# Kernel optimization log

Hardware: AMD Instinct MI355X
Metric: run time of the kernel (lower is better)

## Reference

```python
import jax, jax.numpy as jnp
import numpy as np

N, E = 50000, 800000
F_NODE, F_EDGE, H, LAT, MAXN = 128, 16, 128, 64, 200


def setup_inputs() -> dict:
    key = jax.random.key(0)
    ks = jax.random.split(key, 40)
    s = 0.05
    p = {
        'x': jax.random.normal(ks[0], (N, F_NODE), jnp.float32),
        'edge_index': jax.random.randint(ks[1], (2, E), 0, N, jnp.int64),
        'edge_attr': jax.random.normal(ks[2], (E, F_EDGE), jnp.float32),
        'eps': jax.random.normal(ks[3], (1, LAT), jnp.float32),
        'num_nodes': N,
        # GATConv layer 1 (heads=1)
        'W1': jax.random.normal(ks[4], (F_NODE, H), jnp.float32) * s,
        'att_src1': jax.random.normal(ks[5], (H,), jnp.float32) * s,
        'att_dst1': jax.random.normal(ks[6], (H,), jnp.float32) * s,
        'We1': jax.random.normal(ks[7], (F_EDGE, H), jnp.float32) * s,
        'att_e1': jax.random.normal(ks[8], (H,), jnp.float32) * s,
        'b1': jnp.zeros((H,), jnp.float32),
        # GATConv layer 2
        'W2': jax.random.normal(ks[9], (H, H), jnp.float32) * s,
        'att_src2': jax.random.normal(ks[10], (H,), jnp.float32) * s,
        'att_dst2': jax.random.normal(ks[11], (H,), jnp.float32) * s,
        'We2': jax.random.normal(ks[12], (F_EDGE, H), jnp.float32) * s,
        'att_e2': jax.random.normal(ks[13], (H,), jnp.float32) * s,
        'b2': jnp.zeros((H,), jnp.float32),
        # heads
        'mu_W': jax.random.normal(ks[14], (H, LAT), jnp.float32) * s,
        'mu_b': jnp.zeros((LAT,), jnp.float32),
        'lv_W': jax.random.normal(ks[15], (H, LAT), jnp.float32) * s,
        'lv_b': jnp.zeros((LAT,), jnp.float32),
        'dec_W': jax.random.normal(ks[16], (LAT, H), jnp.float32) * s,
        'dec_b': jnp.zeros((H,), jnp.float32),
        'adj_W1': jax.random.normal(ks[17], (H, H), jnp.float32) * s,
        'adj_b1': jnp.zeros((H,), jnp.float32),
        'adj_W2': jax.random.normal(ks[18], (H, MAXN), jnp.float32) * s,
        'adj_b2': jnp.zeros((MAXN,), jnp.float32),
        'nd_W1': jax.random.normal(ks[19], (H, H), jnp.float32) * s,
        'nd_b1': jnp.zeros((H,), jnp.float32),
        'nd_W2': jax.random.normal(ks[20], (H, F_NODE), jnp.float32) * s,
        'nd_b2': jnp.zeros((F_NODE,), jnp.float32),
    }
    return p


def _gat(h, src, dst, ea, W, a_s, a_d, We, a_e, b, n):
    # PyG GATConv, heads=1: linear transform, per-edge attention, segment softmax over dst
    g = h @ W                                     # [n, H]
    alpha = jax.nn.leaky_relu((g @ a_s)[src] + (g @ a_d)[dst] + (ea @ We) @ a_e,
                              negative_slope=0.2)  # [E']
    m = jax.ops.segment_max(alpha, dst, num_segments=n)
    ex = jnp.exp(alpha - m[dst])
    den = jax.ops.segment_sum(ex, dst, num_segments=n)
    w = ex / den[dst]
    return jax.ops.segment_sum(w[:, None] * g[src], dst, num_segments=n) + b


def _forward(x, edge_index, edge_attr, eps, num_nodes,
             W1, att_src1, att_dst1, We1, att_e1, b1,
             W2, att_src2, att_dst2, We2, att_e2, b2,
             mu_W, mu_b, lv_W, lv_b, dec_W, dec_b,
             adj_W1, adj_b1, adj_W2, adj_b2, nd_W1, nd_b1, nd_W2, nd_b2):
    n = x.shape[0]
    src, dst = edge_index[0], edge_index[1]
    # add self loops; self-loop edge_attr = per-node mean of incoming edge_attr (PyG fill_value='mean')
    deg = jax.ops.segment_sum(jnp.ones((src.shape[0],), x.dtype), dst, num_segments=n)
    mean_ea = jax.ops.segment_sum(edge_attr, dst, num_segments=n) / jnp.maximum(deg, 1.0)[:, None]
    loop = jnp.arange(n)
    src_f = jnp.concatenate([src, loop])
    dst_f = jnp.concatenate([dst, loop])
    ea_f = jnp.concatenate([edge_attr, mean_ea])
    h = jax.nn.relu(_gat(x, src_f, dst_f, ea_f, W1, att_src1, att_dst1, We1, att_e1, b1, n))
    h = jax.nn.relu(_gat(h, src_f, dst_f, ea_f, W2, att_src2, att_dst2, We2, att_e2, b2, n))
    hg = h.mean(axis=0, keepdims=True)            # global_mean_pool, single graph -> [1, H]
    mu = hg @ mu_W + mu_b
    logvar = hg @ lv_W + lv_b
    z = mu + eps * jnp.exp(0.5 * logvar)
    hd = jax.nn.relu(z @ dec_W + dec_b)           # [1, H]
    hn = jnp.broadcast_to(hd[:, None, :], (1, num_nodes, hd.shape[-1]))
    adj = jax.nn.relu(hn @ adj_W1 + adj_b1) @ adj_W2 + adj_b2   # [1, n, MAXN]
    adj = adj[:, :, :num_nodes]
    nodes = jax.nn.relu(hn @ nd_W1 + nd_b1) @ nd_W2 + nd_b2     # [1, n, F_NODE]
    return adj, nodes, mu, logvar


def reference(x, edge_index, edge_attr, eps, num_nodes,
              W1, att_src1, att_dst1, We1, att_e1, b1,
              W2, att_src2, att_dst2, We2, att_e2, b2,
              mu_W, mu_b, lv_W, lv_b, dec_W, dec_b,
              adj_W1, adj_b1, adj_W2, adj_b2, nd_W1, nd_b1, nd_W2, nd_b2):
    return _forward(x, edge_index, edge_attr, eps, num_nodes,
                    W1, att_src1, att_dst1, We1, att_e1, b1,
                    W2, att_src2, att_dst2, We2, att_e2, b2,
                    mu_W, mu_b, lv_W, lv_b, dec_W, dec_b,
                    adj_W1, adj_b1, adj_W2, adj_b2, nd_W1, nd_b1, nd_W2, nd_b2)
```

## Files before the change

kernel.cpp:

```cpp
#include <hip/hip_runtime.h>
#include <math.h>

#define NN   50000
#define EE   800000
#define EF   850000
#define HH   128
#define FE   16
#define LATD 64
#define MAXNN 200

#define ADJ_TOT   10000000
#define NODES_TOT 6400000
#define OUT_TOT   16400000
#define MU_OFF    16400000
#define LV_OFF    16400064

#define GEMMBLOCKS 782
#define DEGBLOCKS  782
#define NBSCAN     49

typedef __attribute__((ext_vector_type(8))) short bf16x8;
typedef __attribute__((ext_vector_type(4))) float f32x4;
typedef __attribute__((ext_vector_type(2))) float f32x2;

__device__ __forceinline__ unsigned short f2bf(float f){
  unsigned int u = __float_as_uint(f);
  unsigned int r = (u + 0x7FFFu + ((u>>16)&1u)) >> 16;
  return (unsigned short)r;
}
__device__ __forceinline__ float bf2f(unsigned short h){
  return __uint_as_float(((unsigned int)h)<<16);
}

__global__ __launch_bounds__(256) void kprep(int* ideg, float* hgsum,
                       const float* We1, const float* ae1, const float* We2, const float* ae2,
                       float* wa1, float* wa2,
                       const float* W1, const float* W2,
                       unsigned short* Wp1, unsigned short* Wp2){
  int i = blockIdx.x*256 + threadIdx.x;
  if(i < NN) ideg[i]=0;
  if(i < HH) hgsum[i]=0.f;
  if(i < FE){
    float s1=0.f, s2=0.f;
    for(int j=0;j<HH;j++){ s1 += We1[i*HH+j]*ae1[j]; s2 += We2[i*HH+j]*ae2[j]; }
    wa1[i]=s1; wa2[i]=s2;
  }
  if(i < HH*HH){
    int n = i >> 7, k = i & 127;
    Wp1[i] = f2bf(W1[k*HH + n]);
    Wp2[i] = f2bf(W2[k*HH + n]);
  }
}

__device__ __forceinline__ void gemm_body(int bid, int tid, const void* __restrict__ hin, int h_is_fp32,
    const unsigned short* __restrict__ Wp,
    const float* __restrict__ atts, const float* __restrict__ attd,
    unsigned char* __restrict__ A8, float* __restrict__ asrc, float* __restrict__ adst){
  int lane = tid & 63;
  int wid  = tid >> 6;
  int l = lane & 15, q = lane >> 4;
  int r0 = bid*64 + wid*16;
  if(r0 >= NN) return;
  const unsigned short* hb = (const unsigned short*)hin;
  const float*          hf = (const float*)hin;
  int row = r0 + l;

  bf16x8 afr[4];
  if(h_is_fp32){
    float4 u[8];
    #pragma unroll
    for(int kb=0;kb<4;kb++){
      const float* p = hf + (size_t)row*HH + kb*32 + q*8;
      u[kb*2]   = *(const float4*)(p);
      u[kb*2+1] = *(const float4*)(p+4);
    }
    #pragma unroll
    for(int kb=0;kb<4;kb++){
      afr[kb][0]=(short)f2bf(u[kb*2].x);   afr[kb][1]=(short)f2bf(u[kb*2].y);
      afr[kb][2]=(short)f2bf(u[kb*2].z);   afr[kb][3]=(short)f2bf(u[kb*2].w);
      afr[kb][4]=(short)f2bf(u[kb*2+1].x); afr[kb][5]=(short)f2bf(u[kb*2+1].y);
      afr[kb][6]=(short)f2bf(u[kb*2+1].z); afr[kb][7]=(short)f2bf(u[kb*2+1].w);
    }
  } else {
    #pragma unroll
    for(int kb=0;kb<4;kb++)
      afr[kb] = *(const bf16x8*)(hb + (size_t)row*HH + kb*32 + q*8);
  }

  f32x4 acc[8];
  #pragma unroll
  for(int t=0;t<8;t++) acc[t]=(f32x4){0.f,0.f,0.f,0.f};

  #pragma unroll
  for(int kb=0;kb<4;kb++){
    #pragma unroll
    for(int t=0;t<8;t++){
      bf16x8 b = *(const bf16x8*)(Wp + (size_t)(t*16+l)*HH + kb*32 + q*8);
      acc[t] = __builtin_amdgcn_mfma_f32_16x16x32_bf16(afr[kb], b, acc[t], 0,0,0);
    }
  }

  float av[8], dv[8];
  #pragma unroll
  for(int t=0;t<8;t++){ av[t]=atts[t*16+l]; dv[t]=attd[t*16+l]; }
  #pragma unroll
  for(int reg=0;reg<4;reg++){
    float ps=0.f, pd=0.f;
    #pragma unroll
    for(int t=0;t<8;t++){ ps+=acc[t][reg]*av[t]; pd+=acc[t][reg]*dv[t]; }
    #pragma unroll
    for(int m=8;m>=1;m>>=1){ ps+=__shfl_xor(ps,m,16); pd+=__shfl_xor(pd,m,16); }
    if(l==0){ int R=r0+q*4+reg; asrc[R]=ps; adst[R]=pd; }
  }
  #pragma unroll
  for(int t=0;t<8;t++)
    #pragma unroll
    for(int reg=0;reg<4;reg++){
      int pk = __builtin_amdgcn_cvt_pk_fp8_f32(acc[t][reg], 0.f, 0, false);
      A8[(size_t)(r0+q*4+reg)*HH + t*16 + l] = (unsigned char)(pk & 0xFF);
    }
}

__global__ __launch_bounds__(256) void kgemm3(const void* __restrict__ hin, int h_is_fp32,
    const unsigned short* __restrict__ Wp,
    const float* __restrict__ atts, const float* __restrict__ attd,
    unsigned char* __restrict__ A8, float* __restrict__ asrc, float* __restrict__ adst){
  gemm_body(blockIdx.x, threadIdx.x, hin, h_is_fp32, Wp, atts, attd, A8, asrc, adst);
}

__global__ __launch_bounds__(256) void kdeggemm(
    const int* __restrict__ ei, int* ideg, unsigned short* __restrict__ erank,
    const void* __restrict__ hin, int h_is_fp32,
    const unsigned short* __restrict__ Wp,
    const float* __restrict__ atts, const float* __restrict__ attd,
    unsigned char* __restrict__ A8, float* __restrict__ asrc, float* __restrict__ adst){
  if(blockIdx.x < GEMMBLOCKS){
    gemm_body(blockIdx.x, threadIdx.x, hin, h_is_fp32, Wp, atts, attd, A8, asrc, adst);
  } else {
    int e0 = ((blockIdx.x - GEMMBLOCKS)*256 + threadIdx.x)*4;
    if(e0 + 3 < EE){
      int4 d4 = *(const int4*)(ei + EE + e0);
      unsigned short r0 = (unsigned short)atomicAdd(&ideg[d4.x], 1);
      unsigned short r1 = (unsigned short)atomicAdd(&ideg[d4.y], 1);
      unsigned short r2 = (unsigned short)atomicAdd(&ideg[d4.z], 1);
      unsigned short r3 = (unsigned short)atomicAdd(&ideg[d4.w], 1);
      ushort4 rr; rr.x=r0; rr.y=r1; rr.z=r2; rr.w=r3;
      *(ushort4*)(erank + e0) = rr;
    } else {
      for(int j=0;j<4;j++)
        if(e0+j < EE) erank[e0+j] = (unsigned short)atomicAdd(&ideg[ei[EE+e0+j]], 1);
    }
  }
}

__global__ void kscan1(const int* __restrict__ ideg, int* rowstart, int* blocksum){
  __shared__ int sd[1024];
  int t=threadIdx.x; int i=blockIdx.x*1024+t;
  int v = (i<NN)? (ideg[i]+1) : 0;
  sd[t]=v; __syncthreads();
  for(int off=1; off<1024; off<<=1){
    int x = (t>=off)? sd[t-off] : 0;
    __syncthreads();
    sd[t] += x;
    __syncthreads();
  }
  if(i<NN) rowstart[i] = sd[t]-v;
  if(t==1023) blocksum[blockIdx.x]=sd[1023];
}
__global__ __launch_bounds__(256) void kscan3i(int* rowstart, const int* __restrict__ blocksum){
  __shared__ int bo[64];
  int t = threadIdx.x;
  if(t < 64){
    int v = (t < NBSCAN)? blocksum[t] : 0;
    int inc = v;
    #pragma unroll
    for(int off=1; off<64; off<<=1){
      int x = __shfl_up(inc, off);
      if(t>=off) inc += x;
    }
    bo[t] = inc - v;
  }
  __syncthreads();
  int i = blockIdx.x*256 + t;
  if(i<NN) rowstart[i] += bo[i>>10];
  if(i==0) rowstart[NN] = bo[NBSCAN];
}

__device__ __forceinline__ unsigned etpack(const float4* a4,
                         const float* __restrict__ wa1, const float* __restrict__ wa2){
  float4 v0=a4[0], v1=a4[1], v2=a4[2], v3=a4[3];
  float va[16]={v0.x,v0.y,v0.z,v0.w, v1.x,v1.y,v1.z,v1.w,
                v2.x,v2.y,v2.z,v2.w, v3.x,v3.y,v3.z,v3.w};
  float d1=0.f,d2=0.f;
  #pragma unroll
  for(int f=0;f<FE;f++){ d1+=va[f]*wa1[f]; d2+=va[f]*wa2[f]; }
  return (unsigned)f2bf(d1) | ((unsigned)f2bf(d2)<<16);
}
__global__ __launch_bounds__(256) void kscatter(const int* __restrict__ ei, const float* __restrict__ ea,
                         const float* __restrict__ wa1, const float* __restrict__ wa2,
                         const int* __restrict__ rowstart, const unsigned short* __restrict__ erank,
                         uint2* __restrict__ csr){
  int e0 = (blockIdx.x*256 + threadIdx.x)*2;
  if(e0>=EE) return;
  int sA=ei[e0],    sB=ei[e0+1];
  int dA=ei[EE+e0], dB=ei[EE+e0+1];
  int rA=(int)erank[e0], rB=(int)erank[e0+1];
  int pA=rowstart[dA]+rA, pB=rowstart[dB]+rB;
  const float4* a4 = (const float4*)(ea + (size_t)e0*FE);
  unsigned yA = etpack(a4,   wa1, wa2);
  unsigned yB = etpack(a4+4, wa1, wa2);
  uint2 enA; enA.x=(unsigned)sA; enA.y=yA;
  uint2 enB; enB.x=(unsigned)sB; enB.y=yB;
  csr[pA]=enA; csr[pB]=enB;
}

__global__ __launch_bounds__(256) void kgat(const unsigned char* __restrict__ A8,
    const float* __restrict__ asrc, const float* __restrict__ adst,
    const int* __restrict__ rowstart, uint2* __restrict__ csr,
    int mode, const float* __restrict__ bias,
    float* __restrict__ alphabuf, int* __restrict__ srcbuf,
    unsigned short* __restrict__ Bout){
  int lane = threadIdx.x & 63;
  int wid  = threadIdx.x >> 6;
  int half = lane >> 5;
  int hl   = lane & 31;
  int i = blockIdx.x*8 + wid*2 + half;
  if(i >= NN) return;
  int base = rowstart[i];
  int len  = rowstart[i+1]-base;
  float adi = adst[i];
  int lq = hl & 15;
  int qq = hl >> 4;
  float av[8];
  #pragma unroll
  for(int j=0;j<8;j++) av[j]=0.f;

  if(__builtin_expect(len <= 32, 1)){
    int P2 = (len+1)>>1;
    int nread = mode ? len : len-1;
    int s = i; float etlo = 0.f, ethi = 0.f;
    if(hl < nread){
      uint2 en = csr[base+hl];
      s = (int)en.x;
      etlo = bf2f((unsigned short)(en.y & 0xFFFFu));
      ethi = bf2f((unsigned short)(en.y >> 16));
    }
    float et = mode ? ethi : etlo;
    int skv0[6];
    #pragma unroll
    for(int j=0;j<6;j++) skv0[j] = (j<P2) ? __shfl(s, 2*j+qq, 32) : i;
    unsigned ux[6], uy[6];
    #pragma unroll
    for(int j=0;j<6;j++){
      uint2 u = *(const uint2*)(A8 + (size_t)skv0[j]*HH + lq*8);
      ux[j]=u.x; uy[j]=u.y;
    }
    if(!mode){
      float e1 = (hl < len-1) ? etlo : 0.f;
      float e2 = (hl < len-1) ? ethi : 0.f;
      #pragma unroll
      for(int mk=16;mk>=1;mk>>=1){ e1 += __shfl_xor(e1,mk); e2 += __shfl_xor(e2,mk); }
      float dg = fmaxf((float)(len-1), 1.f);
      float m1 = e1/dg, m2 = e2/dg;
      if(hl == len-1){
        et = m1;
        uint2 se; se.x=(unsigned)i;
        se.y=(unsigned)f2bf(m1) | ((unsigned)f2bf(m2)<<16);
        csr[base+len-1] = se;
      }
    }
    float a = -1e30f;
    if(hl < len){
      a = asrc[s] + adi + et;
      a = fmaxf(a, 0.2f*a);
    }
    float m = a;
    #pragma unroll
    for(int mk=16;mk>=1;mk>>=1) m = fmaxf(m, __shfl_xor(m,mk));
    float ex = (hl<len) ? __expf(a-m) : 0.f;
    float sm = ex;
    #pragma unroll
    for(int mk=16;mk>=1;mk>>=1) sm += __shfl_xor(sm,mk);
    ex *= __builtin_amdgcn_rcpf(sm);

    float w0[6];
    #pragma unroll
    for(int j=0;j<6;j++) w0[j] = (j<P2) ? __shfl(ex, 2*j+qq, 32) : 0.f;
    #pragma unroll
    for(int j=0;j<6;j++){
      f32x2 v;
      v=__builtin_amdgcn_cvt_pk_f32_fp8((int)ux[j],false); av[0]+=w0[j]*v[0]; av[1]+=w0[j]*v[1];
      v=__builtin_amdgcn_cvt_pk_f32_fp8((int)ux[j],true ); av[2]+=w0[j]*v[0]; av[3]+=w0[j]*v[1];
      v=__builtin_amdgcn_cvt_pk_f32_fp8((int)uy[j],false); av[4]+=w0[j]*v[0]; av[5]+=w0[j]*v[1];
      v=__builtin_amdgcn_cvt_pk_f32_fp8((int)uy[j],true ); av[6]+=w0[j]*v[0]; av[7]+=w0[j]*v[1];
    }
    for(int t0=6; t0<P2; t0+=6){
      int skv[6]; float w[6];
      #pragma unroll
      for(int j=0;j<6;j++){
        if(t0+j < P2){
          int idx = 2*(t0+j) + qq;
          skv[j] = __shfl(s, idx, 32);
          w[j]   = __shfl(ex, idx, 32);
        } else { skv[j] = i; w[j] = 0.f; }
      }
      unsigned vx[6], vy[6];
      #pragma unroll
      for(int j=0;j<6;j++){
        uint2 u = *(const uint2*)(A8 + (size_t)skv[j]*HH + lq*8);
        vx[j]=u.x; vy[j]=u.y;
      }
      #pragma unroll
      for(int j=0;j<6;j++){
        f32x2 v;
        v=__builtin_amdgcn_cvt_pk_f32_fp8((int)vx[j],false); av[0]+=w[j]*v[0]; av[1]+=w[j]*v[1];
        v=__builtin_amdgcn_cvt_pk_f32_fp8((int)vx[j],true ); av[2]+=w[j]*v[0]; av[3]+=w[j]*v[1];
        v=__builtin_amdgcn_cvt_pk_f32_fp8((int)vy[j],false); av[4]+=w[j]*v[0]; av[5]+=w[j]*v[1];
        v=__builtin_amdgcn_cvt_pk_f32_fp8((int)vy[j],true ); av[6]+=w[j]*v[0]; av[7]+=w[j]*v[1];
      }
    }
  } else {
    int deg = len-1;
    int lim = mode ? len : deg;
    float lm = -1e30f, e1 = 0.f, e2 = 0.f;
    for(int k=hl;k<lim;k+=32){
      uint2 en = csr[base+k];
      int sr = (int)en.x;
      float lo = bf2f((unsigned short)(en.y & 0xFFFFu));
      float hi = bf2f((unsigned short)(en.y >> 16));
      float etv = mode ? hi : lo;
      if(!mode){ e1 += lo; e2 += hi; }
      float a = asrc[sr] + adi + etv;
      a = fmaxf(a, 0.2f*a);
      alphabuf[base+k]=a; srcbuf[base+k]=sr;
      lm = fmaxf(lm,a);
    }
    #pragma unroll
    for(int mk=16;mk>=1;mk>>=1){
      e1 += __shfl_xor(e1,mk);
      e2 += __shfl_xor(e2,mk);
      lm  = fmaxf(lm, __shfl_xor(lm,mk));
    }
    float aself = 0.f;
    if(!mode){
      float m1 = e1/(float)deg, m2 = e2/(float)deg;
      aself = asrc[i] + adi + m1;
      aself = fmaxf(aself, 0.2f*aself);
      lm = fmaxf(lm, aself);
      if(hl==0){
        uint2 se; se.x=(unsigned)i;
        se.y=(unsigned)f2bf(m1) | ((unsigned)f2bf(m2)<<16);
        csr[base+deg] = se;
      }
    }
    float ls=0.f;
    for(int k=hl;k<len;k+=32){
      float a;
      if(mode) a = alphabuf[base+k];
      else     a = (k<deg)? alphabuf[base+k] : aself;
      float e_ = __expf(a-lm);
      alphabuf[base+k]=e_;
      ls += e_;
    }
    #pragma unroll
    for(int mk=16;mk>=1;mk>>=1) ls += __shfl_xor(ls,mk);
    float inv = 1.f/ls;
    int lim2 = mode ? len : deg;
    int P2 = (len+1)>>1;
    for(int t=0;t<P2;t++){
      int k = 2*t + qq;
      int sk = i; float wk = 0.f;
      if(k<len){
        sk = (k<lim2)? srcbuf[base+k] : i;
        wk = alphabuf[base+k]*inv;
      }
      uint2 u = *(const uint2*)(A8 + (size_t)sk*HH + lq*8);
      f32x2 v;
      v=__builtin_amdgcn_cvt_pk_f32_fp8((int)u.x,false); av[0]+=wk*v[0]; av[1]+=wk*v[1];
      v=__builtin_amdgcn_cvt_pk_f32_fp8((int)u.x,true ); av[2]+=wk*v[0]; av[3]+=wk*v[1];
      v=__builtin_amdgcn_cvt_pk_f32_fp8((int)u.y,false); av[4]+=wk*v[0]; av[5]+=wk*v[1];
      v=__builtin_amdgcn_cvt_pk_f32_fp8((int)u.y,true ); av[6]+=wk*v[0]; av[7]+=wk*v[1];
    }
  }

  #pragma unroll
  for(int j=0;j<8;j++) av[j] += __shfl_xor(av[j],16);
  if(qq==0){
    const float4* bp = (const float4*)(bias + lq*8);
    float4 b0=bp[0], b1=bp[1];
    float o0=fmaxf(av[0]+b0.x,0.f), o1=fmaxf(av[1]+b0.y,0.f);
    float o2=fmaxf(av[2]+b0.z,0.f), o3=fmaxf(av[3]+b0.w,0.f);
    float o4=fmaxf(av[4]+b1.x,0.f), o5=fmaxf(av[5]+b1.y,0.f);
    float o6=fmaxf(av[6]+b1.z,0.f), o7=fmaxf(av[7]+b1.w,0.f);
    uint4 ov;
    ov.x=(unsigned)f2bf(o0)|((unsigned)f2bf(o1)<<16);
    ov.y=(unsigned)f2bf(o2)|((unsigned)f2bf(o3)<<16);
    ov.z=(unsigned)f2bf(o4)|((unsigned)f2bf(o5)<<16);
    ov.w=(unsigned)f2bf(o6)|((unsigned)f2bf(o7)<<16);
    *(uint4*)(Bout + (size_t)i*HH + lq*8) = ov;
  }
}

__global__ __launch_bounds__(256) void khg(const unsigned short* __restrict__ B, float* hgsum){
  int f = threadIdx.x & 127;
  int half = threadIdx.x >> 7;
  float s=0.f;
  for(int i = blockIdx.x*2+half; i < NN; i += gridDim.x*2)
    s += bf2f(B[(size_t)i*HH + f]);
  __shared__ float sd[256];
  sd[threadIdx.x]=s; __syncthreads();
  if(half==0) atomicAdd(&hgsum[f], sd[threadIdx.x]+sd[threadIdx.x+128]);
}

__global__ __launch_bounds__(256) void kdec(const float* __restrict__ hgsum, const float* __restrict__ eps,
   const float* muW,const float* mub,const float* lvW,const float* lvb,
   const float* decW,const float* decb,
   const float* aW1,const float* ab1,const float* aW2,const float* ab2,
   const float* nW1,const float* nb1,const float* nW2,const float* nb2,
   float* out, float* rowadj, float* rownodes){
  __shared__ float hg[HH], z[LATD], hd[HH], t1[HH], t2[HH];
  int t=threadIdx.x;
  if(t<HH) hg[t]=hgsum[t]*(1.0f/NN);
  __syncthreads();
  if(t<LATD){
    float mu=mub[t], lv=lvb[t];
    #pragma unroll 8
    for(int k=0;k<HH;k++){ mu += hg[k]*muW[k*LATD+t]; lv += hg[k]*lvW[k*LATD+t]; }
    out[MU_OFF+t]=mu; out[LV_OFF+t]=lv;
    z[t]=mu + eps[t]*expf(0.5f*lv);
  }
  __syncthreads();
  if(t<HH){
    float a=decb[t];
    #pragma unroll 8
    for(int k=0;k<LATD;k++) a += z[k]*decW[k*HH+t];
    hd[t]=fmaxf(a,0.f);
  }
  __syncthreads();
  if(t<HH){
    float a=ab1[t];
    #pragma unroll 8
    for(int k=0;k<HH;k++) a += hd[k]*aW1[k*HH+t];
    t1[t]=fmaxf(a,0.f);
  } else {
    int j=t-HH;
    float a=nb1[j];
    #pragma unroll 8
    for(int k=0;k<HH;k++) a += hd[k]*nW1[k*HH+j];
    t2[j]=fmaxf(a,0.f);
  }
  __syncthreads();
  for(int j=t;j<MAXNN;j+=256){
    float a=ab2[j];
    #pragma unroll 8
    for(int k=0;k<HH;k++) a += t1[k]*aW2[k*MAXNN+j];
    rowadj[j]=a;
  }
  if(t<HH){
    float a=nb2[t];
    #pragma unroll 8
    for(int k=0;k<HH;k++) a += t2[k]*nW2[k*HH+t];
    rownodes[t]=a;
  }
}

__global__ __launch_bounds__(256) void kbcast(const float* __restrict__ rowadj,
                                              const float* __restrict__ rownodes,
                                              float* __restrict__ out){
  __shared__ float row[MAXNN+HH];
  int t=threadIdx.x;
  if(t<MAXNN) row[t]=rowadj[t];
  if(t<HH) row[MAXNN+t]=rownodes[t];
  __syncthreads();
  int stride=gridDim.x*blockDim.x;
  const int tot4 = OUT_TOT/4;
  for(int q=blockIdx.x*blockDim.x+t; q<tot4; q+=stride){
    int idx = q*4;
    float4 vv;
    if(idx<ADJ_TOT){
      int j = idx % MAXNN;
      vv = *(const float4*)&row[j];
    } else {
      int j = (idx-ADJ_TOT) & (HH-1);
      vv = *(const float4*)&row[MAXNN+j];
    }
    *(float4*)&out[idx] = vv;
  }
}

extern "C" void kernel_launch(void* const* d_in, const int* in_sizes, int n_in,
                              void* d_out, int out_size, void* d_ws, size_t ws_size,
                              hipStream_t stream){
  const float* x   = (const float*)d_in[0];
  const int*   ei  = (const int*)d_in[1];
  const float* ea  = (const float*)d_in[2];
  const float* eps = (const float*)d_in[3];
  const float* W1  =(const float*)d_in[5];
  const float* as1 =(const float*)d_in[6];
  const float* ad1 =(const float*)d_in[7];
  const float* We1 =(const float*)d_in[8];
  const float* ae1 =(const float*)d_in[9];
  const float* b1  =(const float*)d_in[10];
  const float* W2  =(const float*)d_in[11];
  const float* as2 =(const float*)d_in[12];
  const float* ad2 =(const float*)d_in[13];
  const float* We2 =(const float*)d_in[14];
  const float* ae2 =(const float*)d_in[15];
  const float* b2  =(const float*)d_in[16];
  const float* muW =(const float*)d_in[17];
  const float* mub =(const float*)d_in[18];
  const float* lvW =(const float*)d_in[19];
  const float* lvb =(const float*)d_in[20];
  const float* decW=(const float*)d_in[21];
  const float* decb=(const float*)d_in[22];
  const float* aW1 =(const float*)d_in[23];
  const float* ab1 =(const float*)d_in[24];
  const float* aW2 =(const float*)d_in[25];
  const float* ab2 =(const float*)d_in[26];
  const float* nW1 =(const float*)d_in[27];
  const float* nb1 =(const float*)d_in[28];
  const float* nW2 =(const float*)d_in[29];
  const float* nb2 =(const float*)d_in[30];
  float* out=(float*)d_out;

  char* w=(char*)d_ws;
  unsigned char*  A8  = (unsigned char*)w;  w += (size_t)NN*HH;
  unsigned short* Bbf = (unsigned short*)w; w += (size_t)NN*HH*2;
  unsigned short* Wp1 = (unsigned short*)w; w += (size_t)HH*HH*2;
  unsigned short* Wp2 = (unsigned short*)w; w += (size_t)HH*HH*2;
  uint2*  csr      = (uint2*)w;  w += (size_t)EF*8;
  float*  alphabuf = (float*)w;  w += (size_t)EF*4;
  int*    srcbuf   = (int*)w;    w += (size_t)EF*4;
  unsigned short* erank = (unsigned short*)w; w += (size_t)EE*2;
  int*    rowstart = (int*)w;    w += (size_t)(NN+1)*4;
  int*    ideg     = (int*)w;    w += (size_t)NN*4;
  float*  hgsum    = (float*)w;  w += 128*4;
  float*  asrc     = (float*)w;  w += (size_t)NN*4;
  float*  adst     = (float*)w;  w += (size_t)NN*4;
  float*  wa1      = (float*)w;  w += 16*4;
  float*  wa2      = (float*)w;  w += 16*4;
  float*  rowadj   = (float*)w;  w += 256*4;
  float*  rownodes = (float*)w;  w += 128*4;
  int*    blocksum = (int*)w;    w += 64*4;

  int gatblocks  = (NN+7)/8;

  hipLaunchKernelGGL(kprep, dim3((NN+255)/256), dim3(256), 0, stream,
                     ideg, hgsum, We1, ae1, We2, ae2, wa1, wa2, W1, W2, Wp1, Wp2);
  hipLaunchKernelGGL(kdeggemm, dim3(GEMMBLOCKS+DEGBLOCKS), dim3(256), 0, stream,
                     ei, ideg, erank,
                     (const void*)x, 1, Wp1, as1, ad1, A8, asrc, adst);
  hipLaunchKernelGGL(kscan1, dim3(NBSCAN), dim3(1024), 0, stream, ideg, rowstart, blocksum);
  hipLaunchKernelGGL(kscan3i, dim3((NN+255)/256), dim3(256), 0, stream, rowstart, blocksum);
  hipLaunchKernelGGL(kscatter, dim3((EE/2+255)/256), dim3(256), 0, stream,
                     ei, ea, wa1, wa2, rowstart, erank, csr);
  hipLaunchKernelGGL(kgat,  dim3(gatblocks), dim3(256), 0, stream,
                     A8, asrc, adst, rowstart, csr, 0, b1, alphabuf, srcbuf, Bbf);
  hipLaunchKernelGGL(kgemm3, dim3(GEMMBLOCKS), dim3(256), 0, stream,
                     (const void*)Bbf, 0, Wp2, as2, ad2, A8, asrc, adst);
  hipLaunchKernelGGL(kgat,  dim3(gatblocks), dim3(256), 0, stream,
                     A8, asrc, adst, rowstart, csr, 1, b2, alphabuf, srcbuf, Bbf);
  hipLaunchKernelGGL(khg,   dim3(512), dim3(256), 0, stream, Bbf, hgsum);
  hipLaunchKernelGGL(kdec,  dim3(1), dim3(256), 0, stream, hgsum, eps,
                     muW,mub,lvW,lvb,decW,decb,aW1,ab1,aW2,ab2,nW1,nb1,nW2,nb2,
                     out, rowadj, rownodes);
  hipLaunchKernelGGL(kbcast, dim3(2048), dim3(256), 0, stream, rowadj, rownodes, out);
}
```

Measured before the change: 403.3 us.

## Fuse scan passes, precompute edge terms in degree pass, widen scatter and broadcast

Edge-attribute attention dot products move into the degree-counting blocks of the fused gemm/degree kernel and are stored in a new per-edge buffer, so the scatter kernel only gathers packed values and now handles four edges per thread. The two-pass prefix scan becomes a single kernel in which blocks publish flagged block sums and spin until all other blocks have published, removing one launch. The broadcast kernel is rewritten to write whole rows per wavefront without modulo indexing. The tradeoffs are an extra 3.2 MB write and read for the edge buffer, and an inter-block spin that depends on all 49 scan blocks being resident at the same time. The tail fallback in the degree pass is also removed, which is safe only because EE is divisible by four.

```diff
diff --git a/kernel.cpp b/kernel.cpp
--- a/kernel.cpp
+++ b/kernel.cpp
@@ -18,6 +18,7 @@
 #define GEMMBLOCKS 782
 #define DEGBLOCKS  782
 #define NBSCAN     49
+#define FLAGBIT    0x80000000u
 
 typedef __attribute__((ext_vector_type(8))) short bf16x8;
 typedef __attribute__((ext_vector_type(4))) float f32x4;
@@ -32,7 +33,7 @@
   return __uint_as_float(((unsigned int)h)<<16);
 }
 
-__global__ __launch_bounds__(256) void kprep(int* ideg, float* hgsum,
+__global__ __launch_bounds__(256) void kprep(int* ideg, float* hgsum, unsigned* scanpub,
                        const float* We1, const float* ae1, const float* We2, const float* ae2,
                        float* wa1, float* wa2,
                        const float* W1, const float* W2,
@@ -40,6 +41,7 @@
   int i = blockIdx.x*256 + threadIdx.x;
   if(i < NN) ideg[i]=0;
   if(i < HH) hgsum[i]=0.f;
+  if(i < 64) scanpub[i]=0u;
   if(i < FE){
     float s1=0.f, s2=0.f;
     for(int j=0;j<HH;j++){ s1 += We1[i*HH+j]*ae1[j]; s2 += We2[i*HH+j]*ae2[j]; }
@@ -128,8 +130,21 @@
   gemm_body(blockIdx.x, threadIdx.x, hin, h_is_fp32, Wp, atts, attd, A8, asrc, adst);
 }
 
+__device__ __forceinline__ unsigned etpack(const float4* a4,
+                         const float* __restrict__ wa1, const float* __restrict__ wa2){
+  float4 v0=a4[0], v1=a4[1], v2=a4[2], v3=a4[3];
+  float va[16]={v0.x,v0.y,v0.z,v0.w, v1.x,v1.y,v1.z,v1.w,
+                v2.x,v2.y,v2.z,v2.w, v3.x,v3.y,v3.z,v3.w};
+  float d1=0.f,d2=0.f;
+  #pragma unroll
+  for(int f=0;f<FE;f++){ d1+=va[f]*wa1[f]; d2+=va[f]*wa2[f]; }
+  return (unsigned)f2bf(d1) | ((unsigned)f2bf(d2)<<16);
+}
+
 __global__ __launch_bounds__(256) void kdeggemm(
     const int* __restrict__ ei, int* ideg, unsigned short* __restrict__ erank,
+    const float* __restrict__ ea, const float* __restrict__ wa1, const float* __restrict__ wa2,
+    unsigned* __restrict__ ety,
     const void* __restrict__ hin, int h_is_fp32,
     const unsigned short* __restrict__ Wp,
     const float* __restrict__ atts, const float* __restrict__ attd,
@@ -144,74 +159,66 @@
       unsigned short r1 = (unsigned short)atomicAdd(&ideg[d4.y], 1);
       unsigned short r2 = (unsigned short)atomicAdd(&ideg[d4.z], 1);
       unsigned short r3 = (unsigned short)atomicAdd(&ideg[d4.w], 1);
+      const float4* a4 = (const float4*)(ea + (size_t)e0*FE);
+      uint4 y;
+      y.x = etpack(a4,    wa1, wa2);
+      y.y = etpack(a4+4,  wa1, wa2);
+      y.z = etpack(a4+8,  wa1, wa2);
+      y.w = etpack(a4+12, wa1, wa2);
+      *(uint4*)(ety + e0) = y;
       ushort4 rr; rr.x=r0; rr.y=r1; rr.z=r2; rr.w=r3;
       *(ushort4*)(erank + e0) = rr;
-    } else {
-      for(int j=0;j<4;j++)
-        if(e0+j < EE) erank[e0+j] = (unsigned short)atomicAdd(&ideg[ei[EE+e0+j]], 1);
-    }
-  }
-}
-
-__global__ void kscan1(const int* __restrict__ ideg, int* rowstart, int* blocksum){
+    }
+  }
+}
+
+__global__ void kscanf(const int* __restrict__ ideg, int* __restrict__ rowstart,
+                       unsigned* __restrict__ scanpub){
   __shared__ int sd[1024];
-  int t=threadIdx.x; int i=blockIdx.x*1024+t;
+  __shared__ int bo[64];
+  int t=threadIdx.x, b=blockIdx.x;
+  int i = b*1024 + t;
   int v = (i<NN)? (ideg[i]+1) : 0;
   sd[t]=v; __syncthreads();
   for(int off=1; off<1024; off<<=1){
-    int x = (t>=off)? sd[t-off] : 0;
-    __syncthreads();
-    sd[t] += x;
-    __syncthreads();
-  }
-  if(i<NN) rowstart[i] = sd[t]-v;
-  if(t==1023) blocksum[blockIdx.x]=sd[1023];
-}
-__global__ __launch_bounds__(256) void kscan3i(int* rowstart, const int* __restrict__ blocksum){
-  __shared__ int bo[64];
-  int t = threadIdx.x;
-  if(t < 64){
-    int v = (t < NBSCAN)? blocksum[t] : 0;
-    int inc = v;
+    int x=(t>=off)? sd[t-off]:0; __syncthreads();
+    sd[t]+=x; __syncthreads();
+  }
+  if(t==1023) atomicExch(&scanpub[b], (unsigned)sd[1023] | FLAGBIT);
+  if(t<64){
+    int j = (t<NBSCAN)? t : NBSCAN-1;
+    unsigned u;
+    do { u = atomicAdd(&scanpub[j], 0u); } while(!(u & FLAGBIT));
+    int agg = (t<NBSCAN)? (int)(u & ~FLAGBIT) : 0;
+    int inc = agg;
     #pragma unroll
     for(int off=1; off<64; off<<=1){
       int x = __shfl_up(inc, off);
       if(t>=off) inc += x;
     }
-    bo[t] = inc - v;
+    bo[t] = inc - agg;
   }
   __syncthreads();
-  int i = blockIdx.x*256 + t;
-  if(i<NN) rowstart[i] += bo[i>>10];
-  if(i==0) rowstart[NN] = bo[NBSCAN];
-}
-
-__device__ __forceinline__ unsigned etpack(const float4* a4,
-                         const float* __restrict__ wa1, const float* __restrict__ wa2){
-  float4 v0=a4[0], v1=a4[1], v2=a4[2], v3=a4[3];
-  float va[16]={v0.x,v0.y,v0.z,v0.w, v1.x,v1.y,v1.z,v1.w,
-                v2.x,v2.y,v2.z,v2.w, v3.x,v3.y,v3.z,v3.w};
-  float d1=0.f,d2=0.f;
-  #pragma unroll
-  for(int f=0;f<FE;f++){ d1+=va[f]*wa1[f]; d2+=va[f]*wa2[f]; }
-  return (unsigned)f2bf(d1) | ((unsigned)f2bf(d2)<<16);
-}
-__global__ __launch_bounds__(256) void kscatter(const int* __restrict__ ei, const float* __restrict__ ea,
-                         const float* __restrict__ wa1, const float* __restrict__ wa2,
-                         const int* __restrict__ rowstart, const unsigned short* __restrict__ erank,
+  if(i<NN) rowstart[i] = sd[t]-v + bo[b];
+  if(b==0 && t==0) rowstart[NN] = bo[NBSCAN];
+}
+
+__global__ __launch_bounds__(256) void kscatter(const int* __restrict__ ei,
+                         const unsigned* __restrict__ ety,
+                         const int* __restrict__ rowstart,
+                         const unsigned short* __restrict__ erank,
                          uint2* __restrict__ csr){
-  int e0 = (blockIdx.x*256 + threadIdx.x)*2;
-  if(e0>=EE) return;
-  int sA=ei[e0],    sB=ei[e0+1];
-  int dA=ei[EE+e0], dB=ei[EE+e0+1];
-  int rA=(int)erank[e0], rB=(int)erank[e0+1];
-  int pA=rowstart[dA]+rA, pB=rowstart[dB]+rB;
-  const float4* a4 = (const float4*)(ea + (size_t)e0*FE);
-  unsigned yA = etpack(a4,   wa1, wa2);
-  unsigned yB = etpack(a4+4, wa1, wa2);
-  uint2 enA; enA.x=(unsigned)sA; enA.y=yA;
-  uint2 enB; enB.x=(unsigned)sB; enB.y=yB;
-  csr[pA]=enA; csr[pB]=enB;
+  int e0 = (blockIdx.x*256 + threadIdx.x)*4;
+  if(e0 >= EE) return;
+  int4 s4 = *(const int4*)(ei + e0);
+  int4 d4 = *(const int4*)(ei + EE + e0);
+  ushort4 r4 = *(const ushort4*)(erank + e0);
+  uint4 y4 = *(const uint4*)(ety + e0);
+  uint2 en;
+  en.x=(unsigned)s4.x; en.y=y4.x; csr[rowstart[d4.x]+(int)r4.x]=en;
+  en.x=(unsigned)s4.y; en.y=y4.y; csr[rowstart[d4.y]+(int)r4.y]=en;
+  en.x=(unsigned)s4.z; en.y=y4.z; csr[rowstart[d4.z]+(int)r4.z]=en;
+  en.x=(unsigned)s4.w; en.y=y4.w; csr[rowstart[d4.w]+(int)r4.w]=en;
 }
 
 __global__ __launch_bounds__(256) void kgat(const unsigned char* __restrict__ A8,
@@ -467,25 +474,16 @@
 __global__ __launch_bounds__(256) void kbcast(const float* __restrict__ rowadj,
                                               const float* __restrict__ rownodes,
                                               float* __restrict__ out){
-  __shared__ float row[MAXNN+HH];
-  int t=threadIdx.x;
-  if(t<MAXNN) row[t]=rowadj[t];
-  if(t<HH) row[MAXNN+t]=rownodes[t];
-  __syncthreads();
-  int stride=gridDim.x*blockDim.x;
-  const int tot4 = OUT_TOT/4;
-  for(int q=blockIdx.x*blockDim.x+t; q<tot4; q+=stride){
-    int idx = q*4;
-    float4 vv;
-    if(idx<ADJ_TOT){
-      int j = idx % MAXNN;
-      vv = *(const float4*)&row[j];
-    } else {
-      int j = (idx-ADJ_TOT) & (HH-1);
-      vv = *(const float4*)&row[MAXNN+j];
-    }
-    *(float4*)&out[idx] = vv;
-  }
+  int lane = threadIdx.x & 63;
+  int wv = (blockIdx.x*256 + threadIdx.x) >> 6;
+  int nw = (gridDim.x*256) >> 6;
+  float4 aseg = {0.f,0.f,0.f,0.f}, nseg = {0.f,0.f,0.f,0.f};
+  if(lane<50) aseg = ((const float4*)rowadj)[lane];
+  if(lane<32) nseg = ((const float4*)rownodes)[lane];
+  for(int r=wv; r<NN; r+=nw)
+    if(lane<50) *(float4*)(out + (size_t)r*MAXNN + lane*4) = aseg;
+  for(int r=wv; r<NN; r+=nw)
+    if(lane<32) *(float4*)(out + ADJ_TOT + (size_t)r*HH + lane*4) = nseg;
 }
 
 extern "C" void kernel_launch(void* const* d_in, const int* in_sizes, int n_in,
@@ -531,6 +529,7 @@
   uint2*  csr      = (uint2*)w;  w += (size_t)EF*8;
   float*  alphabuf = (float*)w;  w += (size_t)EF*4;
   int*    srcbuf   = (int*)w;    w += (size_t)EF*4;
+  unsigned* ety    = (unsigned*)w; w += (size_t)EE*4;
   unsigned short* erank = (unsigned short*)w; w += (size_t)EE*2;
   int*    rowstart = (int*)w;    w += (size_t)(NN+1)*4;
   int*    ideg     = (int*)w;    w += (size_t)NN*4;
@@ -541,19 +540,18 @@
   float*  wa2      = (float*)w;  w += 16*4;
   float*  rowadj   = (float*)w;  w += 256*4;
   float*  rownodes = (float*)w;  w += 128*4;
-  int*    blocksum = (int*)w;    w += 64*4;
+  unsigned* scanpub= (unsigned*)w; w += 64*4;
 
   int gatblocks  = (NN+7)/8;
 
   hipLaunchKernelGGL(kprep, dim3((NN+255)/256), dim3(256), 0, stream,
-                     ideg, hgsum, We1, ae1, We2, ae2, wa1, wa2, W1, W2, Wp1, Wp2);
+                     ideg, hgsum, scanpub, We1, ae1, We2, ae2, wa1, wa2, W1, W2, Wp1, Wp2);
   hipLaunchKernelGGL(kdeggemm, dim3(GEMMBLOCKS+DEGBLOCKS), dim3(256), 0, stream,
-                     ei, ideg, erank,
+                     ei, ideg, erank, ea, wa1, wa2, ety,
                      (const void*)x, 1, Wp1, as1, ad1, A8, asrc, adst);
-  hipLaunchKernelGGL(kscan1, dim3(NBSCAN), dim3(1024), 0, stream, ideg, rowstart, blocksum);
-  hipLaunchKernelGGL(kscan3i, dim3((NN+255)/256), dim3(256), 0, stream, rowstart, blocksum);
-  hipLaunchKernelGGL(kscatter, dim3((EE/2+255)/256), dim3(256), 0, stream,
-                     ei, ea, wa1, wa2, rowstart, erank, csr);
+  hipLaunchKernelGGL(kscanf, dim3(NBSCAN), dim3(1024), 0, stream, ideg, rowstart, scanpub);
+  hipLaunchKernelGGL(kscatter, dim3((EE/4+255)/256), dim3(256), 0, stream,
+                     ei, ety, rowstart, erank, csr);
   hipLaunchKernelGGL(kgat,  dim3(gatblocks), dim3(256), 0, stream,
                      A8, asrc, adst, rowstart, csr, 0, b1, alphabuf, srcbuf, Bbf);
   hipLaunchKernelGGL(kgemm3, dim3(GEMMBLOCKS), dim3(256), 0, stream,
```

Result: no change. 399.0 us (-1.1%).
